# Performance work log

Measured on AMD Instinct MI355X. Metric: run time of the kernel, lower is better.

## Reference

```python
import jax, jax.numpy as jnp
import numpy as np

LORA_RANK = 16
LORA_ALPHA = 32
CHUNK_SIZE = 64
TTT_LR = 0.01
SCALING = LORA_ALPHA / LORA_RANK  # 2.0

B, S = 2, 2048
K_DIM, H_DIM = 11008, 4096
EMBED_DIM, VOCAB = 4096, 32000


def setup_inputs() -> dict:
    key = jax.random.key(0)
    ks = jax.random.split(key, 7)
    x = jax.random.normal(ks[0], (B, S, K_DIM), jnp.float32) * 0.02
    input_ids = jax.random.randint(ks[1], (B, S), 0, VOCAB)
    W_base = jax.random.normal(ks[2], (H_DIM, K_DIM), jnp.float32) * 0.02
    embed_table = jax.random.normal(ks[3], (VOCAB, EMBED_DIM), jnp.float32) * 0.02
    W_proj = jax.random.normal(ks[4], (H_DIM, EMBED_DIM), jnp.float32) * 0.02
    init_A = jax.random.normal(ks[5], (H_DIM, LORA_RANK), jnp.float32) * 0.02
    init_B = jax.random.normal(ks[6], (LORA_RANK, K_DIM), jnp.float32) * 0.02
    return dict(x=x, W_base=W_base, embed_table=embed_table, W_proj=W_proj,
                init_A=init_A, init_B=init_B, input_ids=input_ids)


def reference(x, W_base, embed_table, W_proj, init_A, init_B, input_ids):
    # base (frozen) linear: x [B,S,k] @ W_base^T [k,h]
    base_out = jnp.einsum('bsk,hk->bsh', x, W_base)

    # TTT targets: embedding of NEXT token (shift-by-1, zero-padded), frozen lookup
    embeds = embed_table[input_ids]  # [B,S,E]
    shifted = jnp.concatenate([embeds[:, 1:, :], jnp.zeros_like(embeds[:, :1, :])], axis=1)
    V = jnp.einsum('bse,he->bsh', shifted, W_proj)  # [B,S,h]

    Bsz, Seq, k = x.shape
    h = W_base.shape[0]
    pad = (-Seq) % CHUNK_SIZE
    Zp = jnp.pad(x, ((0, 0), (0, pad), (0, 0)))
    Vp = jnp.pad(V, ((0, 0), (0, pad), (0, 0)))
    nc = Zp.shape[1] // CHUNK_SIZE
    Z = Zp.reshape(Bsz, nc, CHUNK_SIZE, k)    # [B,N,C,k]
    Vc = Vp.reshape(Bsz, nc, CHUNK_SIZE, h)   # [B,N,C,h]

    # per-chunk fast updates
    # dA = V^T @ (Z @ B^T) : [B,N,h,r]
    proj_in = jnp.einsum('bnck,rk->bncr', Z, init_B)
    dA = jnp.einsum('bnch,bncr->bnhr', Vc, proj_in)
    # dB = (V @ A)^T @ Z : [B,N,r,k]
    proj_err = jnp.einsum('bnch,hr->bncr', Vc, init_A)
    dB = jnp.einsum('bncr,bnck->bnrk', proj_err, Z)

    # exclusive prefix-sum over chunks (chunk i sees updates from chunks < i)
    csA = jnp.cumsum(dA, axis=1)
    csB = jnp.cumsum(dB, axis=1)
    accA = jnp.concatenate([jnp.zeros_like(csA[:, :1]), csA[:, :-1]], axis=1)
    accB = jnp.concatenate([jnp.zeros_like(csB[:, :1]), csB[:, :-1]], axis=1)

    lr = TTT_LR * SCALING
    A_eff = init_A[None, None] - lr * accA  # [B,N,h,r]
    B_eff = init_B[None, None] - lr * accB  # [B,N,r,k]

    mid = jnp.einsum('bnck,bnrk->bncr', Z, B_eff)
    lora = jnp.einsum('bncr,bnhr->bnch', mid, A_eff)  # [B,N,C,h]
    lora = lora.reshape(Bsz, nc * CHUNK_SIZE, h)[:, :Seq]
    return base_out + lora * SCALING
```

## Files before the change

kernel.cpp:

```cpp
#include <hip/hip_runtime.h>

typedef __attribute__((ext_vector_type(8))) short bf16x8;
typedef __attribute__((ext_vector_type(4))) float f32x4;

__device__ __forceinline__ float b2f(short s) {
  return __uint_as_float(((unsigned int)(unsigned short)s) << 16);
}
__device__ __forceinline__ short f2b(float f) {
  unsigned int u = __float_as_uint(f);
  unsigned int r = (u + 0x7fffu + ((u >> 16) & 1u)) >> 16;
  return (short)(unsigned short)r;
}

#define GLOAD16(g, l) __builtin_amdgcn_global_load_lds( \
    (const __attribute__((address_space(1))) void*)(g),  \
    (__attribute__((address_space(3))) void*)(l), 16, 0, 0)

__global__ __launch_bounds__(256) void cvt_kernel(const float* __restrict__ src,
                                                  short* __restrict__ dst, long n) {
  long i = ((long)blockIdx.x * 256 + threadIdx.x) * 8;
  long stride = (long)gridDim.x * 256 * 8;
  for (; i + 8 <= n; i += stride) {
    float4 a = *(const float4*)(src + i);
    float4 b = *(const float4*)(src + i + 4);
    bf16x8 o;
    o[0] = f2b(a.x); o[1] = f2b(a.y); o[2] = f2b(a.z); o[3] = f2b(a.w);
    o[4] = f2b(b.x); o[5] = f2b(b.y); o[6] = f2b(b.z); o[7] = f2b(b.w);
    *(bf16x8*)(dst + i) = o;
  }
}

__global__ __launch_bounds__(256) void gather_kernel(const float* __restrict__ emb,
    const int* __restrict__ ids, short* __restrict__ sh) {
  const int token = blockIdx.x;
  const int s = token & 2047;
  const long dst = (long)token * 4096;
  const int row = (s == 2047) ? -1 : ids[token + 1];
  for (int it = 0; it < 2; ++it) {
    const int e = it * 2048 + threadIdx.x * 8;
    bf16x8 o;
    if (row < 0) {
      #pragma unroll
      for (int j = 0; j < 8; ++j) o[j] = 0;
    } else {
      float4 a = *(const float4*)(emb + (long)row * 4096 + e);
      float4 b = *(const float4*)(emb + (long)row * 4096 + e + 4);
      o[0] = f2b(a.x); o[1] = f2b(a.y); o[2] = f2b(a.z); o[3] = f2b(a.w);
      o[4] = f2b(b.x); o[5] = f2b(b.y); o[6] = f2b(b.z); o[7] = f2b(b.w);
    }
    *(bf16x8*)(sh + dst + e) = o;
  }
}

__global__ __launch_bounds__(256) void tposeA_kernel(const float* __restrict__ A,
                                                     short* __restrict__ At) {
  const int h = blockIdx.x * 256 + threadIdx.x;
  #pragma unroll
  for (int r = 0; r < 16; ++r) At[(long)r * 4096 + h] = f2b(A[(long)h * 16 + r]);
}

template <int OUTBF16>
__global__ __launch_bounds__(512, 2) void gemm8p(const short* __restrict__ A,
    const short* __restrict__ B, void* __restrict__ C, int M, int N, int Kd) {
  __shared__ short lds[65536];
  const int tid = threadIdx.x;
  const int lane = tid & 63;
  const int wid = tid >> 6;
  const int wr = wid >> 2;
  const int wcn = wid & 3;
  const int l15 = lane & 15, l4 = lane >> 4, l7 = lane & 7;
  const int lb = (lane >> 3) & 1;

  const int nbx = N >> 8;
  const int cpx = gridDim.x >> 3;
  const int wg = ((int)blockIdx.x & 7) * cpx + ((int)blockIdx.x >> 3);
  const long m0 = (long)(wg / nbx) * 256;
  const long n0 = (long)(wg % nbx) * 256;

  const int NT = Kd >> 6;

  const int rho = lane >> 3;
  const short* Ag = A + (m0 + wid * 8 + rho) * (long)Kd + (l7 ^ rho) * 8;
  const short* Bg = B + (n0 + wid * 8 + rho) * (long)Kd + (l7 ^ rho) * 8;

#define STAGE_A(b, kt, c) GLOAD16(Ag + (long)(c) * 64 * Kd + (long)(kt) * 64, \
    (char*)lds + (b) * 65536 + ((c) * 8 + wid) * 1024 + lane * 16)
#define STAGE_B(b, kt, c) GLOAD16(Bg + (long)(c) * 64 * Kd + (long)(kt) * 64, \
    (char*)lds + (b) * 65536 + 32768 + ((c) * 8 + wid) * 1024 + lane * 16)

  int aLane[2];
  #pragma unroll
  for (int h = 0; h < 2; ++h)
    aLane[h] = (lb * 64 + l7 * 8 + ((h * 4 + l4) ^ l7)) * 16;

#define READ_A(dst, buf, c)                                                   \
  do {                                                                        \
    _Pragma("unroll")                                                         \
    for (int sub = 0; sub < 2; ++sub) {                                       \
      dst[sub][0] = *(const bf16x8*)((buf) + (c) * 8192 + wr * 4096 +         \
                                     sub * 2048 + aLane[0]);                  \
      dst[sub][1] = *(const bf16x8*)((buf) + (c) * 8192 + wr * 4096 +         \
                                     sub * 2048 + aLane[1]);                  \
    }                                                                         \
  } while (0)

#define READ_B(buf)                                                           \
  do {                                                                        \
    _Pragma("unroll")                                                         \
    for (int nf = 0; nf < 4; ++nf) {                                          \
      bv[nf][0] = *(const bf16x8*)((buf) + 32768 + wcn * 8192 + nf * 2048 +   \
                                   aLane[0]);                                 \
      bv[nf][1] = *(const bf16x8*)((buf) + 32768 + wcn * 8192 + nf * 2048 +   \
                                   aLane[1]);                                 \
    }                                                                         \
  } while (0)

#define MFMA_BLOCK(q, av)                                                     \
  do {                                                                        \
    _Pragma("unroll")                                                         \
    for (int sub = 0; sub < 2; ++sub)                                         \
      _Pragma("unroll")                                                       \
      for (int nf = 0; nf < 4; ++nf) {                                        \
        acc[(q) * 2 + sub][nf] = __builtin_amdgcn_mfma_f32_16x16x32_bf16(     \
            av[sub][0], bv[nf][0], acc[(q) * 2 + sub][nf], 0, 0, 0);          \
        acc[(q) * 2 + sub][nf] = __builtin_amdgcn_mfma_f32_16x16x32_bf16(     \
            av[sub][1], bv[nf][1], acc[(q) * 2 + sub][nf], 0, 0, 0);          \
      }                                                                       \
  } while (0)

  f32x4 acc[8][4];
  #pragma unroll
  for (int m = 0; m < 8; ++m)
    #pragma unroll
    for (int n = 0; n < 4; ++n) {
      acc[m][n][0] = 0.f; acc[m][n][1] = 0.f;
      acc[m][n][2] = 0.f; acc[m][n][3] = 0.f;
    }

  STAGE_A(0, 0, 0); STAGE_B(0, 0, 0);
  STAGE_A(0, 0, 1); STAGE_B(0, 0, 1);
  STAGE_A(0, 0, 2); STAGE_B(0, 0, 2);
  STAGE_A(0, 0, 3); STAGE_B(0, 0, 3);
  STAGE_A(1, 1, 0); STAGE_B(1, 1, 0);
  STAGE_A(1, 1, 1); STAGE_B(1, 1, 1);
  STAGE_A(1, 1, 2); STAGE_B(1, 1, 2);
  asm volatile("s_waitcnt vmcnt(6)" ::: "memory");
  __builtin_amdgcn_s_barrier();
  asm volatile("" ::: "memory");

  const char* ldsb = (const char*)lds;
  bf16x8 avX[2][2], avY[2][2], bv[4][2];
  READ_B(ldsb);
  READ_A(avX, ldsb, 0);

  for (int t = 0; t < NT; ++t) {
    const int cur = t & 1;
    const int tn1 = (t + 1 < NT) ? t + 1 : 0;
    const int tn2 = (t + 2 < NT) ? t + 2 : 0;
    const char* pc = ldsb + cur * 65536;
    const char* pn = ldsb + (cur ^ 1) * 65536;

    READ_A(avY, pc, 1);
    STAGE_A(cur ^ 1, tn1, 3); STAGE_B(cur ^ 1, tn1, 3);
    __builtin_amdgcn_s_barrier();
    asm volatile("s_waitcnt lgkmcnt(4)" ::: "memory");
    __builtin_amdgcn_sched_barrier(0);
    __builtin_amdgcn_s_setprio(1);
    MFMA_BLOCK(0, avX);
    __builtin_amdgcn_s_setprio(0);
    __builtin_amdgcn_s_barrier();
    asm volatile("" ::: "memory");

    READ_A(avX, pc, 2);
    STAGE_A(cur, tn2, 0); STAGE_B(cur, tn2, 0);
    __builtin_amdgcn_s_barrier();
    asm volatile("s_waitcnt lgkmcnt(4)" ::: "memory");
    __builtin_amdgcn_sched_barrier(0);
    __builtin_amdgcn_s_setprio(1);
    MFMA_BLOCK(1, avY);
    __builtin_amdgcn_s_setprio(0);
    __builtin_amdgcn_s_barrier();
    asm volatile("" ::: "memory");

    READ_A(avY, pc, 3);
    STAGE_A(cur, tn2, 1); STAGE_B(cur, tn2, 1);
    __builtin_amdgcn_s_barrier();
    asm volatile("s_waitcnt lgkmcnt(4)" ::: "memory");
    __builtin_amdgcn_sched_barrier(0);
    __builtin_amdgcn_s_setprio(1);
    MFMA_BLOCK(2, avX);
    __builtin_amdgcn_s_setprio(0);
    __builtin_amdgcn_s_barrier();
    asm volatile("" ::: "memory");

    STAGE_A(cur, tn2, 2); STAGE_B(cur, tn2, 2);
    asm volatile("s_waitcnt vmcnt(6)" ::: "memory");
    __builtin_amdgcn_s_barrier();
    asm volatile("s_waitcnt lgkmcnt(0)" ::: "memory");
    __builtin_amdgcn_sched_barrier(0);
    __builtin_amdgcn_s_setprio(1);
    MFMA_BLOCK(3, avY);
    __builtin_amdgcn_s_setprio(0);
    __builtin_amdgcn_sched_barrier(0);
    READ_B(pn);
    READ_A(avX, pn, 0);
    __builtin_amdgcn_s_barrier();
    asm volatile("" ::: "memory");
  }
#undef STAGE_A
#undef STAGE_B
#undef READ_A
#undef READ_B
#undef MFMA_BLOCK

  #pragma unroll
  for (int q = 0; q < 4; ++q)
    #pragma unroll
    for (int sub = 0; sub < 2; ++sub)
      #pragma unroll
      for (int nf = 0; nf < 4; ++nf)
        #pragma unroll
        for (int j = 0; j < 4; ++j) {
          const long row = m0 + q * 64 + wr * 32 + sub * 16 + l4 * 4 + j;
          const long col = n0 + wcn * 64 + nf * 16 + l15;
          if (OUTBF16) ((short*)C)[row * N + col] = f2b(acc[q * 2 + sub][nf][j]);
          else         ((float*)C)[row * N + col] = acc[q * 2 + sub][nf][j];
        }
}

__global__ __launch_bounds__(256) void gemv16(const short* __restrict__ A,
    const short* __restrict__ W, float* __restrict__ part, int Kd, int Klen,
    long wStride) {
  __shared__ short lds[8192];
  const int tid = threadIdx.x;
  const int lane = tid & 63;
  const int w = tid >> 6;
  const int l15 = lane & 15, l4 = lane >> 4;
  const int rho = lane >> 3, j7 = lane & 7;
  const long m0 = (long)blockIdx.x * 64;
  const long k0 = (long)blockIdx.y * Klen;
  const int NTk = Klen >> 6;
  const short* Wr = W + (wStride ? (long)blockIdx.x * wStride : 0);
  const short* Ag = A + (m0 + w * 8 + rho) * (long)Kd + k0 + (j7 ^ rho) * 8;

#define STG(b, kt, i) GLOAD16(Ag + (long)(i) * 32 * Kd + (long)(kt) * 64, \
    (char*)lds + (b) * 8192 + ((i) * 4 + w) * 1024 + lane * 16)

  int aOff[2];
  #pragma unroll
  for (int kk = 0; kk < 2; ++kk)
    aOff[kk] = ((w * 16 + l15) >> 3) * 1024 + (l15 & 7) * 128 +
               (((kk * 4 + l4) ^ (l15 & 7)) * 16);

  f32x4 acc; acc[0] = 0.f; acc[1] = 0.f; acc[2] = 0.f; acc[3] = 0.f;

  STG(0, 0, 0); STG(0, 0, 1);
  for (int t = 0; t < NTk; ++t) {
    const int cur = t & 1;
    const int tn = (t + 1 < NTk) ? t + 1 : 0;
    const short* wp = Wr + (long)l15 * Kd + k0 + (long)t * 64 + l4 * 8;
    bf16x8 wv0 = *(const bf16x8*)(wp);
    bf16x8 wv1 = *(const bf16x8*)(wp + 32);
    STG(cur ^ 1, tn, 0); STG(cur ^ 1, tn, 1);
    asm volatile("s_waitcnt vmcnt(2)" ::: "memory");
    __builtin_amdgcn_s_barrier();
    bf16x8 a0 = *(const bf16x8*)((const char*)lds + cur * 8192 + aOff[0]);
    bf16x8 a1 = *(const bf16x8*)((const char*)lds + cur * 8192 + aOff[1]);
    asm volatile("s_waitcnt lgkmcnt(0)" ::: "memory");
    __builtin_amdgcn_sched_barrier(0);
    acc = __builtin_amdgcn_mfma_f32_16x16x32_bf16(a0, wv0, acc, 0, 0, 0);
    acc = __builtin_amdgcn_mfma_f32_16x16x32_bf16(a1, wv1, acc, 0, 0, 0);
    __builtin_amdgcn_s_barrier();
  }
#undef STG

  float* dst = part + (long)blockIdx.y * 65536;
  #pragma unroll
  for (int r = 0; r < 4; ++r)
    dst[(m0 + w * 16 + l4 * 4 + r) * 16 + l15] = acc[r];
}

__global__ __launch_bounds__(256) void reduce4_kernel(const float* __restrict__ s0,
    float* __restrict__ d0, const float* __restrict__ s1, float* __restrict__ d1) {
  const long idx = (long)blockIdx.x * 256 + threadIdx.x;
  const float* s = blockIdx.y ? s1 : s0;
  float* d = blockIdx.y ? d1 : d0;
  d[idx] = s[idx] + s[idx + 65536] + s[idx + 131072] + s[idx + 196608];
}

__global__ __launch_bounds__(256) void dA_kernel(const short* __restrict__ V,
    const float* __restrict__ pin, float* __restrict__ dA) {
  const int chunk = blockIdx.y;
  const int h = blockIdx.x * 256 + threadIdx.x;
  __shared__ float ps[1024];
  #pragma unroll
  for (int i = 0; i < 4; ++i)
    ps[i * 256 + threadIdx.x] = pin[(long)chunk * 1024 + i * 256 + threadIdx.x];
  __syncthreads();
  float acc[16];
  #pragma unroll
  for (int r = 0; r < 16; ++r) acc[r] = 0.f;
  for (int c = 0; c < 64; ++c) {
    const float v = b2f(V[((long)chunk * 64 + c) * 4096 + h]);
    #pragma unroll
    for (int r = 0; r < 16; ++r) acc[r] = fmaf(v, ps[c * 16 + r], acc[r]);
  }
  float* dst = dA + ((long)chunk * 4096 + h) * 16;
  #pragma unroll
  for (int i = 0; i < 4; ++i) {
    f32x4 w; w[0] = acc[i*4]; w[1] = acc[i*4+1]; w[2] = acc[i*4+2]; w[3] = acc[i*4+3];
    *(f32x4*)(dst + i * 4) = w;
  }
}

__global__ __launch_bounds__(256) void dB_kernel(const short* __restrict__ X,
    const float* __restrict__ per, float* __restrict__ dB) {
  const int chunk = blockIdx.y;
  const int k = blockIdx.x * 256 + threadIdx.x;
  __shared__ float ps[1024];
  #pragma unroll
  for (int i = 0; i < 4; ++i)
    ps[i * 256 + threadIdx.x] = per[(long)chunk * 1024 + i * 256 + threadIdx.x];
  __syncthreads();
  float acc[16];
  #pragma unroll
  for (int r = 0; r < 16; ++r) acc[r] = 0.f;
  for (int c = 0; c < 64; ++c) {
    const float xv = b2f(X[((long)chunk * 64 + c) * 11008 + k]);
    #pragma unroll
    for (int r = 0; r < 16; ++r) acc[r] = fmaf(xv, ps[c * 16 + r], acc[r]);
  }
  #pragma unroll
  for (int r = 0; r < 16; ++r)
    dB[((long)chunk * 16 + r) * 11008 + k] = acc[r];
}

__global__ __launch_bounds__(256) void scanA_kernel(const float* __restrict__ dA,
    const float* __restrict__ initA, short* __restrict__ Aeff) {
  const int b = blockIdx.y;
  const long idx = (long)blockIdx.x * 256 + threadIdx.x;
  const float a0 = initA[idx];
  float acc = 0.f;
  for (int n = 0; n < 32; ++n) {
    const long chunk = (long)b * 32 + n;
    Aeff[chunk * 65536 + idx] = f2b(a0 - 0.02f * acc);
    acc += dA[chunk * 65536 + idx];
  }
}

__global__ __launch_bounds__(256) void scanB_kernel(const float* __restrict__ dB,
    const float* __restrict__ initB, short* __restrict__ Beff) {
  const int b = blockIdx.y;
  const long idx = (long)blockIdx.x * 256 + threadIdx.x;
  const float b0 = initB[idx];
  float acc = 0.f;
  for (int n = 0; n < 32; ++n) {
    const long chunk = (long)b * 32 + n;
    Beff[chunk * 176128 + idx] = f2b(b0 - 0.02f * acc);
    acc += dB[chunk * 176128 + idx];
  }
}

__global__ __launch_bounds__(256) void final_kernel(const short* __restrict__ base,
    const float* __restrict__ mid, const short* __restrict__ Aeff,
    float* __restrict__ out) {
  const int token = blockIdx.x;
  const int chunk = token >> 6;
  __shared__ float m[16];
  if (threadIdx.x < 16) m[threadIdx.x] = mid[(long)token * 16 + threadIdx.x];
  __syncthreads();
  float mf[16];
  #pragma unroll
  for (int r = 0; r < 16; ++r) mf[r] = m[r];
  for (int it = 0; it < 2; ++it) {
    const int h0 = it * 2048 + threadIdx.x * 8;
    bf16x8 bs = *(const bf16x8*)(base + (long)token * 4096 + h0);
    float res[8];
    #pragma unroll
    for (int j = 0; j < 8; ++j) {
      const short* ar = Aeff + ((long)chunk * 4096 + h0 + j) * 16;
      bf16x8 a0 = *(const bf16x8*)ar;
      bf16x8 a1 = *(const bf16x8*)(ar + 8);
      float s = 0.f;
      #pragma unroll
      for (int r = 0; r < 8; ++r) {
        s = fmaf(mf[r], b2f(a0[r]), s);
        s = fmaf(mf[r + 8], b2f(a1[r]), s);
      }
      res[j] = b2f(bs[j]) + 2.0f * s;
    }
    #pragma unroll
    for (int i = 0; i < 2; ++i) {
      f32x4 w; w[0] = res[i*4]; w[1] = res[i*4+1]; w[2] = res[i*4+2]; w[3] = res[i*4+3];
      *(f32x4*)(out + (long)token * 4096 + h0 + i * 4) = w;
    }
  }
}

extern "C" void kernel_launch(void* const* d_in, const int* in_sizes, int n_in,
                              void* d_out, int out_size, void* d_ws, size_t ws_size,
                              hipStream_t stream) {
  const float* x     = (const float*)d_in[0];
  const float* Wbase = (const float*)d_in[1];
  const float* emb   = (const float*)d_in[2];
  const float* Wproj = (const float*)d_in[3];
  const float* initA = (const float*)d_in[4];
  const float* initB = (const float*)d_in[5];
  const int*   ids   = (const int*)d_in[6];
  float* outp = (float*)d_out;

  char* p = (char*)d_ws;
  short* xb   = (short*)p; p += 90177536L;
  short* Wb   = (short*)p; p += 90177536L;
  short* Wpb  = (short*)p; p += 33554432L;
  short* shb  = (short*)p; p += 33554432L;
  short* Vb   = (short*)p; p += 33554432L;
  short* base = (short*)p; p += 33554432L;
  short* iBb  = (short*)p; p += 352256L;
  short* iAt  = (short*)p; p += 131072L;
  float* pin  = (float*)p; p += 262144L;
  float* per  = (float*)p; p += 262144L;
  float* mid  = (float*)p; p += 262144L;
  short* Aeff = (short*)p; p += 8388608L;
  short* Beff = (short*)p; p += 22544384L;
  float* pinP = (float*)p; p += 1048576L;
  float* perP = (float*)p; p += 1048576L;
  float* midP = (float*)p; p += 1048576L;
  float* dA = (float*)Wpb;
  float* dB = (float*)((char*)Wpb + 16777216L);

  cvt_kernel<<<2048, 256, 0, stream>>>(x, xb, 45088768L);
  cvt_kernel<<<2048, 256, 0, stream>>>(Wbase, Wb, 45088768L);
  cvt_kernel<<<2048, 256, 0, stream>>>(Wproj, Wpb, 16777216L);
  cvt_kernel<<<86, 256, 0, stream>>>(initB, iBb, 176128L);
  tposeA_kernel<<<16, 256, 0, stream>>>(initA, iAt);
  gather_kernel<<<4096, 256, 0, stream>>>(emb, ids, shb);

  gemm8p<1><<<256, 512, 0, stream>>>(shb, Wpb, (void*)Vb, 4096, 4096, 4096);
  gemm8p<1><<<256, 512, 0, stream>>>(xb, Wb, (void*)base, 4096, 4096, 11008);

  gemv16<<<dim3(64, 4), 256, 0, stream>>>(xb, iBb, pinP, 11008, 2752, 0L);
  gemv16<<<dim3(64, 4), 256, 0, stream>>>(Vb, iAt, perP, 4096, 1024, 0L);
  reduce4_kernel<<<dim3(256, 2), 256, 0, stream>>>(pinP, pin, perP, per);

  dA_kernel<<<dim3(16, 64), 256, 0, stream>>>(Vb, pin, dA);
  dB_kernel<<<dim3(43, 64), 256, 0, stream>>>(xb, per, dB);
  scanA_kernel<<<dim3(256, 2), 256, 0, stream>>>(dA, initA, Aeff);
  scanB_kernel<<<dim3(688, 2), 256, 0, stream>>>(dB, initB, Beff);

  gemv16<<<dim3(64, 4), 256, 0, stream>>>(xb, Beff, midP, 11008, 2752, 176128L);
  reduce4_kernel<<<dim3(256, 1), 256, 0, stream>>>(midP, mid, midP, mid);
  final_kernel<<<4096, 256, 0, stream>>>(base, mid, Aeff, outp);
}
```

Baseline: 759.9 us.

## Merge prep, gemv, dA/dB and scan launches; fold partial-sum reductions into consumers

Combines the six conversion, transpose and gather launches into two grid-stride kernels. Also merges the paired gemv, dA/dB and scan launches into single kernels that branch on block index. The separate reduce4 kernels are removed, so consumers sum the four split-K partials when they read them. This cuts launch count and the gaps between small kernels, at the cost of redundant partial-sum reads per block and branchy mixed-work grids.

```diff
diff --git a/kernel.cpp b/kernel.cpp
--- a/kernel.cpp
+++ b/kernel.cpp
@@ -16,47 +16,63 @@
     (const __attribute__((address_space(1))) void*)(g),  \
     (__attribute__((address_space(3))) void*)(l), 16, 0, 0)
 
-__global__ __launch_bounds__(256) void cvt_kernel(const float* __restrict__ src,
-                                                  short* __restrict__ dst, long n) {
-  long i = ((long)blockIdx.x * 256 + threadIdx.x) * 8;
-  long stride = (long)gridDim.x * 256 * 8;
-  for (; i + 8 <= n; i += stride) {
-    float4 a = *(const float4*)(src + i);
-    float4 b = *(const float4*)(src + i + 4);
+__global__ __launch_bounds__(256) void prep1(const float* __restrict__ x,
+    const float* __restrict__ wb, const float* __restrict__ wp,
+    short* __restrict__ dst) {
+  const long NX = 5636096L, NW = 11272192L, NT = 13369344L;
+  for (long it = (long)blockIdx.x * 256 + threadIdx.x; it < NT;
+       it += (long)gridDim.x * 256) {
+    const float* s; long off;
+    if (it < NX)      { s = x;  off = it; }
+    else if (it < NW) { s = wb; off = it - NX; }
+    else              { s = wp; off = it - NW; }
+    float4 a = *(const float4*)(s + off * 8);
+    float4 b = *(const float4*)(s + off * 8 + 4);
     bf16x8 o;
     o[0] = f2b(a.x); o[1] = f2b(a.y); o[2] = f2b(a.z); o[3] = f2b(a.w);
     o[4] = f2b(b.x); o[5] = f2b(b.y); o[6] = f2b(b.z); o[7] = f2b(b.w);
-    *(bf16x8*)(dst + i) = o;
-  }
-}
-
-__global__ __launch_bounds__(256) void gather_kernel(const float* __restrict__ emb,
-    const int* __restrict__ ids, short* __restrict__ sh) {
-  const int token = blockIdx.x;
-  const int s = token & 2047;
-  const long dst = (long)token * 4096;
-  const int row = (s == 2047) ? -1 : ids[token + 1];
-  for (int it = 0; it < 2; ++it) {
-    const int e = it * 2048 + threadIdx.x * 8;
-    bf16x8 o;
-    if (row < 0) {
-      #pragma unroll
-      for (int j = 0; j < 8; ++j) o[j] = 0;
-    } else {
-      float4 a = *(const float4*)(emb + (long)row * 4096 + e);
-      float4 b = *(const float4*)(emb + (long)row * 4096 + e + 4);
+    *(bf16x8*)(dst + it * 8) = o;
+  }
+}
+
+__global__ __launch_bounds__(256) void prep2(const float* __restrict__ initB,
+    short* __restrict__ iBb, const float* __restrict__ initA,
+    short* __restrict__ iAt, const float* __restrict__ emb,
+    const int* __restrict__ ids, short* __restrict__ shb) {
+  const long N1 = 22016L, N2 = 26112L, NT = 2123264L;
+  for (long it = (long)blockIdx.x * 256 + threadIdx.x; it < NT;
+       it += (long)gridDim.x * 256) {
+    if (it < N1) {
+      float4 a = *(const float4*)(initB + it * 8);
+      float4 b = *(const float4*)(initB + it * 8 + 4);
+      bf16x8 o;
       o[0] = f2b(a.x); o[1] = f2b(a.y); o[2] = f2b(a.z); o[3] = f2b(a.w);
       o[4] = f2b(b.x); o[5] = f2b(b.y); o[6] = f2b(b.z); o[7] = f2b(b.w);
-    }
-    *(bf16x8*)(sh + dst + e) = o;
-  }
-}
-
-__global__ __launch_bounds__(256) void tposeA_kernel(const float* __restrict__ A,
-                                                     short* __restrict__ At) {
-  const int h = blockIdx.x * 256 + threadIdx.x;
-  #pragma unroll
-  for (int r = 0; r < 16; ++r) At[(long)r * 4096 + h] = f2b(A[(long)h * 16 + r]);
+      *(bf16x8*)(iBb + it * 8) = o;
+    } else if (it < N2) {
+      const int h = (int)(it - N1);
+      #pragma unroll
+      for (int r = 0; r < 16; ++r)
+        iAt[(long)r * 4096 + h] = f2b(initA[(long)h * 16 + r]);
+    } else {
+      const long i3 = it - N2;
+      const int token = (int)(i3 >> 9);
+      const int e = ((int)i3 & 511) * 8;
+      const int s = token & 2047;
+      const int row = (s == 2047) ? -1 : ids[token + 1];
+      bf16x8 o;
+      if (row < 0) {
+        #pragma unroll
+        for (int j = 0; j < 8; ++j) o[j] = 0;
+      } else {
+        float4 a = *(const float4*)(emb + (long)row * 4096 + e);
+        float4 b = *(const float4*)(emb + (long)row * 4096 + e + 4);
+        o[0] = f2b(a.x); o[1] = f2b(a.y); o[2] = f2b(a.z); o[3] = f2b(a.w);
+        o[4] = f2b(b.x); o[5] = f2b(b.y); o[6] = f2b(b.z); o[7] = f2b(b.w);
+      }
+      *(bf16x8*)(shb + (long)token * 4096 + e) = o;
+    }
+  }
 }
 
 template <int OUTBF16>
@@ -228,10 +244,9 @@
         }
 }
 
-__global__ __launch_bounds__(256) void gemv16(const short* __restrict__ A,
+__device__ __forceinline__ void gemv_core(short* lds, const short* __restrict__ A,
     const short* __restrict__ W, float* __restrict__ part, int Kd, int Klen,
     long wStride) {
-  __shared__ short lds[8192];
   const int tid = threadIdx.x;
   const int lane = tid & 63;
   const int w = tid >> 6;
@@ -280,94 +295,109 @@
     dst[(m0 + w * 16 + l4 * 4 + r) * 16 + l15] = acc[r];
 }
 
-__global__ __launch_bounds__(256) void reduce4_kernel(const float* __restrict__ s0,
-    float* __restrict__ d0, const float* __restrict__ s1, float* __restrict__ d1) {
-  const long idx = (long)blockIdx.x * 256 + threadIdx.x;
-  const float* s = blockIdx.y ? s1 : s0;
-  float* d = blockIdx.y ? d1 : d0;
-  d[idx] = s[idx] + s[idx + 65536] + s[idx + 131072] + s[idx + 196608];
-}
-
-__global__ __launch_bounds__(256) void dA_kernel(const short* __restrict__ V,
-    const float* __restrict__ pin, float* __restrict__ dA) {
+__global__ __launch_bounds__(256) void gemv_pinper(const short* __restrict__ xb,
+    const short* __restrict__ iBb, float* __restrict__ pinP,
+    const short* __restrict__ Vb, const short* __restrict__ iAt,
+    float* __restrict__ perP) {
+  __shared__ short lds[8192];
+  if (blockIdx.z == 0) gemv_core(lds, xb, iBb, pinP, 11008, 2752, 0L);
+  else                 gemv_core(lds, Vb, iAt, perP, 4096, 1024, 0L);
+}
+
+__global__ __launch_bounds__(256) void gemv_mid(const short* __restrict__ xb,
+    const short* __restrict__ Beff, float* __restrict__ midP) {
+  __shared__ short lds[8192];
+  gemv_core(lds, xb, Beff, midP, 11008, 2752, 176128L);
+}
+
+__global__ __launch_bounds__(256) void dAdB_kernel(const short* __restrict__ V,
+    const short* __restrict__ X, const float* __restrict__ pinP,
+    const float* __restrict__ perP, float* __restrict__ dA,
+    float* __restrict__ dB) {
   const int chunk = blockIdx.y;
-  const int h = blockIdx.x * 256 + threadIdx.x;
   __shared__ float ps[1024];
-  #pragma unroll
-  for (int i = 0; i < 4; ++i)
-    ps[i * 256 + threadIdx.x] = pin[(long)chunk * 1024 + i * 256 + threadIdx.x];
-  __syncthreads();
-  float acc[16];
-  #pragma unroll
-  for (int r = 0; r < 16; ++r) acc[r] = 0.f;
-  for (int c = 0; c < 64; ++c) {
-    const float v = b2f(V[((long)chunk * 64 + c) * 4096 + h]);
-    #pragma unroll
-    for (int r = 0; r < 16; ++r) acc[r] = fmaf(v, ps[c * 16 + r], acc[r]);
-  }
-  float* dst = dA + ((long)chunk * 4096 + h) * 16;
-  #pragma unroll
-  for (int i = 0; i < 4; ++i) {
-    f32x4 w; w[0] = acc[i*4]; w[1] = acc[i*4+1]; w[2] = acc[i*4+2]; w[3] = acc[i*4+3];
-    *(f32x4*)(dst + i * 4) = w;
-  }
-}
-
-__global__ __launch_bounds__(256) void dB_kernel(const short* __restrict__ X,
-    const float* __restrict__ per, float* __restrict__ dB) {
-  const int chunk = blockIdx.y;
-  const int k = blockIdx.x * 256 + threadIdx.x;
-  __shared__ float ps[1024];
-  #pragma unroll
-  for (int i = 0; i < 4; ++i)
-    ps[i * 256 + threadIdx.x] = per[(long)chunk * 1024 + i * 256 + threadIdx.x];
-  __syncthreads();
-  float acc[16];
-  #pragma unroll
-  for (int r = 0; r < 16; ++r) acc[r] = 0.f;
-  for (int c = 0; c < 64; ++c) {
-    const float xv = b2f(X[((long)chunk * 64 + c) * 11008 + k]);
-    #pragma unroll
-    for (int r = 0; r < 16; ++r) acc[r] = fmaf(xv, ps[c * 16 + r], acc[r]);
-  }
-  #pragma unroll
-  for (int r = 0; r < 16; ++r)
-    dB[((long)chunk * 16 + r) * 11008 + k] = acc[r];
-}
-
-__global__ __launch_bounds__(256) void scanA_kernel(const float* __restrict__ dA,
-    const float* __restrict__ initA, short* __restrict__ Aeff) {
+  if (blockIdx.x < 16) {
+    const int h = blockIdx.x * 256 + threadIdx.x;
+    #pragma unroll
+    for (int i = 0; i < 4; ++i) {
+      const long o = (long)chunk * 1024 + i * 256 + threadIdx.x;
+      ps[i * 256 + threadIdx.x] = pinP[o] + pinP[o + 65536] +
+                                  pinP[o + 131072] + pinP[o + 196608];
+    }
+    __syncthreads();
+    float acc[16];
+    #pragma unroll
+    for (int r = 0; r < 16; ++r) acc[r] = 0.f;
+    for (int c = 0; c < 64; ++c) {
+      const float v = b2f(V[((long)chunk * 64 + c) * 4096 + h]);
+      #pragma unroll
+      for (int r = 0; r < 16; ++r) acc[r] = fmaf(v, ps[c * 16 + r], acc[r]);
+    }
+    float* dst = dA + ((long)chunk * 4096 + h) * 16;
+    #pragma unroll
+    for (int i = 0; i < 4; ++i) {
+      f32x4 w; w[0] = acc[i*4]; w[1] = acc[i*4+1]; w[2] = acc[i*4+2]; w[3] = acc[i*4+3];
+      *(f32x4*)(dst + i * 4) = w;
+    }
+  } else {
+    const int k = (blockIdx.x - 16) * 256 + threadIdx.x;
+    #pragma unroll
+    for (int i = 0; i < 4; ++i) {
+      const long o = (long)chunk * 1024 + i * 256 + threadIdx.x;
+      ps[i * 256 + threadIdx.x] = perP[o] + perP[o + 65536] +
+                                  perP[o + 131072] + perP[o + 196608];
+    }
+    __syncthreads();
+    float acc[16];
+    #pragma unroll
+    for (int r = 0; r < 16; ++r) acc[r] = 0.f;
+    for (int c = 0; c < 64; ++c) {
+      const float xv = b2f(X[((long)chunk * 64 + c) * 11008 + k]);
+      #pragma unroll
+      for (int r = 0; r < 16; ++r) acc[r] = fmaf(xv, ps[c * 16 + r], acc[r]);
+    }
+    #pragma unroll
+    for (int r = 0; r < 16; ++r)
+      dB[((long)chunk * 16 + r) * 11008 + k] = acc[r];
+  }
+}
+
+__global__ __launch_bounds__(256) void scan_kernel(const float* __restrict__ dA,
+    const float* __restrict__ initA, short* __restrict__ Aeff,
+    const float* __restrict__ dB, const float* __restrict__ initB,
+    short* __restrict__ Beff) {
   const int b = blockIdx.y;
-  const long idx = (long)blockIdx.x * 256 + threadIdx.x;
-  const float a0 = initA[idx];
-  float acc = 0.f;
-  for (int n = 0; n < 32; ++n) {
-    const long chunk = (long)b * 32 + n;
-    Aeff[chunk * 65536 + idx] = f2b(a0 - 0.02f * acc);
-    acc += dA[chunk * 65536 + idx];
-  }
-}
-
-__global__ __launch_bounds__(256) void scanB_kernel(const float* __restrict__ dB,
-    const float* __restrict__ initB, short* __restrict__ Beff) {
-  const int b = blockIdx.y;
-  const long idx = (long)blockIdx.x * 256 + threadIdx.x;
-  const float b0 = initB[idx];
-  float acc = 0.f;
-  for (int n = 0; n < 32; ++n) {
-    const long chunk = (long)b * 32 + n;
-    Beff[chunk * 176128 + idx] = f2b(b0 - 0.02f * acc);
-    acc += dB[chunk * 176128 + idx];
+  if (blockIdx.x < 256) {
+    const long idx = (long)blockIdx.x * 256 + threadIdx.x;
+    const float a0 = initA[idx];
+    float acc = 0.f;
+    for (int n = 0; n < 32; ++n) {
+      const long chunk = (long)b * 32 + n;
+      Aeff[chunk * 65536 + idx] = f2b(a0 - 0.02f * acc);
+      acc += dA[chunk * 65536 + idx];
+    }
+  } else {
+    const long idx = (long)(blockIdx.x - 256) * 256 + threadIdx.x;
+    const float b0 = initB[idx];
+    float acc = 0.f;
+    for (int n = 0; n < 32; ++n) {
+      const long chunk = (long)b * 32 + n;
+      Beff[chunk * 176128 + idx] = f2b(b0 - 0.02f * acc);
+      acc += dB[chunk * 176128 + idx];
+    }
   }
 }
 
 __global__ __launch_bounds__(256) void final_kernel(const short* __restrict__ base,
-    const float* __restrict__ mid, const short* __restrict__ Aeff,
+    const float* __restrict__ midP, const short* __restrict__ Aeff,
     float* __restrict__ out) {
   const int token = blockIdx.x;
   const int chunk = token >> 6;
   __shared__ float m[16];
-  if (threadIdx.x < 16) m[threadIdx.x] = mid[(long)token * 16 + threadIdx.x];
+  if (threadIdx.x < 16) {
+    const long o = (long)token * 16 + threadIdx.x;
+    m[threadIdx.x] = midP[o] + midP[o + 65536] + midP[o + 131072] + midP[o + 196608];
+  }
   __syncthreads();
   float mf[16];
   #pragma unroll
@@ -418,9 +448,6 @@
   short* base = (short*)p; p += 33554432L;
   short* iBb  = (short*)p; p += 352256L;
   short* iAt  = (short*)p; p += 131072L;
-  float* pin  = (float*)p; p += 262144L;
-  float* per  = (float*)p; p += 262144L;
-  float* mid  = (float*)p; p += 262144L;
   short* Aeff = (short*)p; p += 8388608L;
   short* Beff = (short*)p; p += 22544384L;
   float* pinP = (float*)p; p += 1048576L;
@@ -429,26 +456,16 @@
   float* dA = (float*)Wpb;
   float* dB = (float*)((char*)Wpb + 16777216L);
 
-  cvt_kernel<<<2048, 256, 0, stream>>>(x, xb, 45088768L);
-  cvt_kernel<<<2048, 256, 0, stream>>>(Wbase, Wb, 45088768L);
-  cvt_kernel<<<2048, 256, 0, stream>>>(Wproj, Wpb, 16777216L);
-  cvt_kernel<<<86, 256, 0, stream>>>(initB, iBb, 176128L);
-  tposeA_kernel<<<16, 256, 0, stream>>>(initA, iAt);
-  gather_kernel<<<4096, 256, 0, stream>>>(emb, ids, shb);
+  prep1<<<2048, 256, 0, stream>>>(x, Wbase, Wproj, xb);
+  prep2<<<2048, 256, 0, stream>>>(initB, iBb, initA, iAt, emb, ids, shb);
 
   gemm8p<1><<<256, 512, 0, stream>>>(shb, Wpb, (void*)Vb, 4096, 4096, 4096);
   gemm8p<1><<<256, 512, 0, stream>>>(xb, Wb, (void*)base, 4096, 4096, 11008);
 
-  gemv16<<<dim3(64, 4), 256, 0, stream>>>(xb, iBb, pinP, 11008, 2752, 0L);
-  gemv16<<<dim3(64, 4), 256, 0, stream>>>(Vb, iAt, perP, 4096, 1024, 0L);
-  reduce4_kernel<<<dim3(256, 2), 256, 0, stream>>>(pinP, pin, perP, per);
-
-  dA_kernel<<<dim3(16, 64), 256, 0, stream>>>(Vb, pin, dA);
-  dB_kernel<<<dim3(43, 64), 256, 0, stream>>>(xb, per, dB);
-  scanA_kernel<<<dim3(256, 2), 256, 0, stream>>>(dA, initA, Aeff);
-  scanB_kernel<<<dim3(688, 2), 256, 0, stream>>>(dB, initB, Beff);
-
-  gemv16<<<dim3(64, 4), 256, 0, stream>>>(xb, Beff, midP, 11008, 2752, 176128L);
-  reduce4_kernel<<<dim3(256, 1), 256, 0, stream>>>(midP, mid, midP, mid);
-  final_kernel<<<4096, 256, 0, stream>>>(base, mid, Aeff, outp);
-}
+  gemv_pinper<<<dim3(64, 4, 2), 256, 0, stream>>>(xb, iBb, pinP, Vb, iAt, perP);
+  dAdB_kernel<<<dim3(59, 64), 256, 0, stream>>>(Vb, xb, pinP, perP, dA, dB);
+  scan_kernel<<<dim3(944, 2), 256, 0, stream>>>(dA, initA, Aeff, dB, initB, Beff);
+
+  gemv_mid<<<dim3(64, 4), 256, 0, stream>>>(xb, Beff, midP);
+  final_kernel<<<4096, 256, 0, stream>>>(base, midP, Aeff, outp);
+}
```

After: 732.0 us. 1.04x faster.
